# Kernel optimization log

Measured on AMD Instinct MI355X. Metric: run time of the kernel, lower is better.

Reference implementation:

```python
import jax, jax.numpy as jnp
import numpy as np

D, H, L, FF, V, B, S = 512, 8, 6, 2048, 4096, 2, 4096
EPS = 1e-5

def _unit(v):
    return v / jnp.linalg.norm(v, axis=-1, keepdims=True)

def _unitelu(v):
    return jax.nn.elu(_unit(v))

def _ln(x, g, b):
    m = jnp.mean(x, axis=-1, keepdims=True)
    var = jnp.var(x, axis=-1, keepdims=True)
    return (x - m) * jax.lax.rsqrt(var + EPS) * g + b

def setup_inputs() -> dict:
    key = jax.random.key(0)
    ks = jax.random.split(key, 16)
    s = 0.02
    inp = {
        'input': jax.random.randint(ks[0], (B, S), 0, V),
        'emb': jax.random.normal(ks[1], (V, D)) * s,
        'Wq': jax.random.normal(ks[2], (L, D, D)) * s,
        'bq': jnp.zeros((L, D)),
        'Wk': jax.random.normal(ks[3], (L, D, D)) * s,
        'bk': jnp.zeros((L, D)),
        'Wv': jax.random.normal(ks[4], (L, D, D)) * s,
        'bv': jnp.zeros((L, D)),
        'Wo': jax.random.normal(ks[5], (L, D, D)) * s,
        'bo': jnp.zeros((L, D)),
        'W1': jax.random.normal(ks[6], (L, FF, D)) * s,
        'b1': jnp.zeros((L, FF)),
        'W2': jax.random.normal(ks[7], (L, D, FF)) * s,
        'b2': jnp.zeros((L, D)),
        'g2': jnp.ones((L, D)),
        'be2': jnp.zeros((L, D)),
        'Wfc': jax.random.normal(ks[8], (V, D)) * s,
        'bfc': jnp.zeros((V,)),
    }
    return inp

def reference(input, emb, Wq, bq, Wk, bk, Wv, bv, Wo, bo, W1, b1, W2, b2, g2, be2, Wfc, bfc):
    # h: [S, B, D] (seq-major, matching input.permute(1,0) then embedding)
    h = emb[input.T]
    for l in range(L):
        # linear kernelized attention: O(S * dh^2) per head, no SxS matrix
        k = _unitelu((h @ Wk[l].T + bk[l]).reshape(S, B, H, -1))  # [S,B,H,dh]
        v = (h @ Wv[l].T + bv[l]).reshape(S, B, H, -1)
        A = jnp.einsum('sbnq,sbnv->bnvq', k, v)                    # [B,H,dh,dh]
        q = _unit((h @ Wq[l].T + bq[l]).reshape(S, B, H, -1))
        o = jnp.einsum('sbnq,bnvq->sbnv', q, A).reshape(S, B, D)
        h = h + (o @ Wo[l].T + bo[l])
        f = jax.nn.relu(h @ W1[l].T + b1[l]) @ W2[l].T + b2[l]
        h = _ln(h + f, g2[l], be2[l])
    out = h @ Wfc.T + bfc          # [S, B, V]
    return out.transpose(1, 2, 0)  # [B, V, S]
```

## Files before the change

### kernel.cpp

```cpp
#include <hip/hip_runtime.h>
#include <hip/hip_bf16.h>

#define D_  512
#define H_  8
#define DH_ 64
#define L_  6
#define FF_ 2048
#define V_  4096
#define B_  2
#define S_  4096
#define SB_ (S_*B_)
#define DD_ ((size_t)D_*D_)
#define FD_ ((size_t)FF_*D_)
#define NTOT_ (4*DD_ + 2*FD_)

typedef unsigned short u16;
typedef unsigned int   u32;
typedef _Float16 f16;
typedef f16   f16x8 __attribute__((ext_vector_type(8)));
typedef float f32x4 __attribute__((ext_vector_type(4)));

__device__ __forceinline__ float us2f(u16 u){
  union { u32 i; float f; } c; c.i = ((u32)u) << 16; return c.f;
}
__device__ __forceinline__ u16 f2b(float f){
  union { float f; u32 i; } c; c.f = f;
  u32 x = c.i;
  x += 0x7FFF + ((x >> 16) & 1);
  return (u16)(x >> 16);
}
__device__ __forceinline__ float h2f(u16 u){
  union { u16 s; f16 h; } c; c.s = u; return (float)c.h;
}
__device__ __forceinline__ u16 f2h(float f){
  union { f16 h; u16 s; } c; c.h = (f16)f; return c.s;
}
__device__ __forceinline__ float ldf(const void* p, size_t i, int isbf){
  return isbf ? us2f(((const u16*)p)[i]) : ((const float*)p)[i];
}

typedef const __attribute__((address_space(1))) u32* gas_u32p;
typedef       __attribute__((address_space(3))) u32* las_u32p;
__device__ __forceinline__ void async16(const u16* g, u16* l){
  __builtin_amdgcn_global_load_lds((gas_u32p)(const void*)g, (las_u32p)(void*)l, 16, 0, 0);
}

__global__ __launch_bounds__(64) void detect_dtype(const void* emb, int* flag)
{
  const int t = threadIdx.x;
  u16 hw = ((const u16*)emb)[t];
  int e = (hw >> 7) & 0xFF;
  int ok = ((e > 96) && (e < 160)) || ((hw & 0x7FFF) == 0);
  unsigned long long m = __ballot(ok);
  if (t == 0) *flag = (__popcll(m) >= 56) ? 1 : 0;
}

__global__ __launch_bounds__(256) void cvt_all(
    const void* Wq, const void* Wk, const void* Wv, const void* Wo,
    const void* W1, const void* W2, const void* Wfc,
    u16* __restrict__ dstAll, u16* __restrict__ dstFC, const int* flagp)
{
  const int isbf = *flagp;
  const size_t total6 = 6 * NTOT_;
  const size_t i = ((size_t)blockIdx.x * 256 + threadIdx.x) * 4;
  const void* src; size_t off; u16* dst;
  if (i < total6) {
    const int l = (int)(i / NTOT_);
    const size_t r = i - (size_t)l * NTOT_;
    const size_t n4 = 4 * DD_, nW1 = n4 + FD_;
    if (r < n4) {
      const int wsel = (int)(r / DD_);
      src = (wsel == 0) ? Wq : (wsel == 1) ? Wk : (wsel == 2) ? Wv : Wo;
      off = (size_t)l * DD_ + (r - (size_t)wsel * DD_);
    } else if (r < nW1) { src = W1; off = (size_t)l * FD_ + (r - n4); }
    else                { src = W2; off = (size_t)l * FD_ + (r - nW1); }
    dst = dstAll + i;
  } else {
    const size_t j = i - total6;
    if (j >= (size_t)V_ * D_) return;
    src = Wfc; off = j; dst = dstFC + j;
  }
  ushort4 o;
  if (isbf) {
    ushort4 u = *(const ushort4*)((const u16*)src + off);
    o = make_ushort4(f2h(us2f(u.x)), f2h(us2f(u.y)), f2h(us2f(u.z)), f2h(us2f(u.w)));
  } else {
    float4 f = *(const float4*)((const float*)src + off);
    o = make_ushort4(f2h(f.x), f2h(f.y), f2h(f.z), f2h(f.w));
  }
  *(ushort4*)dst = o;
}

template<int ACT, int OUTMODE, int PRE, int TPB, int LOG_TX, int LOG_TXZ>
__global__ __launch_bounds__(256) void gemm_pers(
    const u16* __restrict__ A, const u16* __restrict__ Bm,
    int bstride,
    const void* bias, size_t bias_off,
    u16* __restrict__ Cb, void* __restrict__ Cout,
    int M, int N, int K, const int* flagp)
{
  __shared__ u16 tile[(PRE + 1) * 8192];
  const int t = threadIdx.x, lane = t & 63, w = t >> 6;
  const int wr = w >> 1, wc = w & 1;
  const int col = lane & 15, quad = lane >> 4;
  const int srow = w * 16 + (lane >> 2);
  const int skol = (((lane & 3) ^ ((lane >> 3) & 3)) << 3);
  const int rswz = ((col >> 1) & 3);
  const int isbf = *flagp;
  const int vbase = blockIdx.x * TPB;

  float bpre3[(OUTMODE == 3) ? 16 : 1];
  float bpre0[(OUTMODE == 3) ? 1 : TPB][4];
  if (OUTMODE == 3) {
    const int by0 = vbase >> LOG_TXZ;
    #pragma unroll
    for (int i = 0; i < 4; i++)
      #pragma unroll
      for (int r = 0; r < 4; r++)
        bpre3[i * 4 + r] = ldf(bias, bias_off + (by0 << 7) + wr * 64 + i * 16 + quad * 4 + r, isbf);
  } else {
    #pragma unroll
    for (int g = 0; g < TPB; g++) {
      const int bxg = (vbase + g) & ((1 << LOG_TX) - 1);
      #pragma unroll
      for (int j = 0; j < 4; j++)
        bpre0[g][j] = ldf(bias, bias_off + (bxg << 7) + wc * 64 + j * 16 + col, isbf);
    }
  }

  int st = -1;
  const u16 *ag0 = nullptr, *ag1 = nullptr, *bg0 = nullptr, *bg1 = nullptr;
  auto set_tile = [&](int tp) {
    const int v  = vbase + tp;
    const int by = v >> LOG_TXZ;
    const int rr = v & ((1 << LOG_TXZ) - 1);
    const int bz = rr >> LOG_TX;
    const int bx = rr & ((1 << LOG_TX) - 1);
    ag0 = A + (size_t)((by << 7) + srow) * K + skol;
    ag1 = ag0 + (size_t)64 * K;
    bg0 = Bm + ((size_t)((bx << 7) + srow) * bstride + bz) * K + skol;
    bg1 = bg0 + (size_t)64 * bstride * K;
  };
  auto stage = [&](int u) {
    const int tp = u >> 4;
    if (tp != st) { st = tp; set_tile(tp); }
    const int k0 = (u & 15) << 5;
    const int bo = (u % (PRE + 1)) * 8192;
    async16(ag0 + k0, &tile[bo +        w * 512]);
    async16(ag1 + k0, &tile[bo + 2048 + w * 512]);
    async16(bg0 + k0, &tile[bo + 4096 + w * 512]);
    async16(bg1 + k0, &tile[bo + 6144 + w * 512]);
  };

  const int U = TPB * 16;
  #pragma unroll
  for (int p = 0; p < PRE; ++p) stage(p);
  if (PRE >= 2) asm volatile("s_waitcnt vmcnt(4)" ::: "memory");
  else          asm volatile("s_waitcnt vmcnt(0)" ::: "memory");
  __builtin_amdgcn_s_barrier();
  asm volatile("" ::: "memory");

  f32x4 acc[4][4] = {};
  for (int u = 0; u < U; ++u) {
    if (u + PRE < U) stage(u + PRE);
    const int cur = (u % (PRE + 1)) * 8192;
    f16x8 af[4], bf[4];
    #pragma unroll
    for (int i = 0; i < 4; i++)
      af[i] = *(const f16x8*)&tile[cur + (wr * 64 + i * 16 + col) * 32 + ((quad ^ rswz) * 8)];
    #pragma unroll
    for (int j = 0; j < 4; j++)
      bf[j] = *(const f16x8*)&tile[cur + 4096 + (wc * 64 + j * 16 + col) * 32 + ((quad ^ rswz) * 8)];
    #pragma unroll
    for (int i = 0; i < 4; i++)
      #pragma unroll
      for (int j = 0; j < 4; j++)
        acc[i][j] = __builtin_amdgcn_mfma_f32_16x16x32_f16(af[i], bf[j], acc[i][j], 0, 0, 0);

    if ((u & 15) == 15) {
      const int v  = vbase + (u >> 4);
      const int by = v >> LOG_TXZ;
      const int rr = v & ((1 << LOG_TXZ) - 1);
      const int bz = rr >> LOG_TX;
      const int bx = rr & ((1 << LOG_TX) - 1);
      const int bm = by << 7, bn = bx << 7;
      if (OUTMODE == 3) {
        const size_t obase = (size_t)bz * M * N;
        #pragma unroll
        for (int i = 0; i < 4; i++)
          #pragma unroll
          for (int r = 0; r < 4; r++) {
            const int m = bm + wr * 64 + i * 16 + quad * 4 + r;
            #pragma unroll
            for (int j = 0; j < 4; j++) {
              const int n = bn + wc * 64 + j * 16 + col;
              const float c = acc[i][j][r] + bpre3[i * 4 + r];
              const size_t oi = obase + (size_t)m * N + n;
              if (isbf) ((u16*)Cout)[oi] = f2b(c);
              else      ((float*)Cout)[oi] = c;
            }
          }
      } else {
        const int g = u >> 4;
        #pragma unroll
        for (int i = 0; i < 4; i++)
          #pragma unroll
          for (int r = 0; r < 4; r++) {
            const int m = bm + wr * 64 + i * 16 + quad * 4 + r;
            #pragma unroll
            for (int j = 0; j < 4; j++) {
              const int n = bn + wc * 64 + j * 16 + col;
              float c = acc[i][j][r] + bpre0[g][j];
              if (ACT == 1) c = fmaxf(c, 0.f);
              Cb[(size_t)m * N + n] = f2h(c);
            }
          }
      }
      const f32x4 z = {0.f, 0.f, 0.f, 0.f};
      #pragma unroll
      for (int i = 0; i < 4; i++)
        #pragma unroll
        for (int j = 0; j < 4; j++)
          acc[i][j] = z;
    }

    if (PRE >= 2 && u + 2 < U) asm volatile("s_waitcnt vmcnt(4)" ::: "memory");
    else                       asm volatile("s_waitcnt vmcnt(0)" ::: "memory");
    __builtin_amdgcn_s_barrier();
    asm volatile("" ::: "memory");
  }
}

template<int ACT, int OUTMODE, int PRE>
__global__ __launch_bounds__(256) void gemm_mfma64(
    const u16* __restrict__ A, const u16* __restrict__ Bm,
    const void* bias, size_t bias_off,
    const float* __restrict__ res,
    float* __restrict__ Cf, u16* __restrict__ Cb,
    int M, int N, int K, const int* flagp)
{
  __shared__ u16 tile[(PRE + 1) * 6144];
  const int t = threadIdx.x, lane = t & 63, w = t >> 6;
  const int bm = blockIdx.y << 6, bn = blockIdx.x << 7;
  const int wr = w >> 1, wc = w & 1;
  const int col = lane & 15, quad = lane >> 4;

  const int srow = w * 16 + (lane >> 2);
  const int skol = (((lane & 3) ^ ((lane >> 3) & 3)) << 3);
  const u16* ag  = A + (size_t)(bm + srow) * K + skol;
  const u16* bg0 = Bm + (size_t)(bn + srow) * K + skol;
  const u16* bg1 = Bm + (size_t)(bn + 64 + srow) * K + skol;
  u16* la  = &tile[       w * 512];
  u16* lb0 = &tile[2048 + w * 512];
  u16* lb1 = &tile[4096 + w * 512];

  const int nt = K >> 5;

  #pragma unroll
  for (int p = 0; p < PRE; ++p) {
    const int k0 = p << 5, bo = p * 6144;
    async16(ag  + k0, la  + bo);
    async16(bg0 + k0, lb0 + bo);
    async16(bg1 + k0, lb1 + bo);
  }
  if      (PRE >= 3) asm volatile("s_waitcnt vmcnt(6)" ::: "memory");
  else if (PRE == 2) asm volatile("s_waitcnt vmcnt(3)" ::: "memory");
  else               asm volatile("s_waitcnt vmcnt(0)" ::: "memory");
  __builtin_amdgcn_s_barrier();
  asm volatile("" ::: "memory");

  const int rswz = ((col >> 1) & 3);

  f32x4 acc[2][4] = {};
  for (int t2 = 0; t2 < nt; ++t2) {
    if (t2 + PRE < nt) {
      const int k0 = (t2 + PRE) << 5;
      const int bo = ((t2 + PRE) % (PRE + 1)) * 6144;
      async16(ag  + k0, la  + bo);
      async16(bg0 + k0, lb0 + bo);
      async16(bg1 + k0, lb1 + bo);
    }
    const int cur = (t2 % (PRE + 1)) * 6144;
    f16x8 af[2], bf[4];
    #pragma unroll
    for (int i = 0; i < 2; i++)
      af[i] = *(const f16x8*)&tile[cur + (wr * 32 + i * 16 + col) * 32 + ((quad ^ rswz) * 8)];
    #pragma unroll
    for (int j = 0; j < 4; j++)
      bf[j] = *(const f16x8*)&tile[cur + 2048 + (wc * 64 + j * 16 + col) * 32 + ((quad ^ rswz) * 8)];
    #pragma unroll
    for (int i = 0; i < 2; i++)
      #pragma unroll
      for (int j = 0; j < 4; j++)
        acc[i][j] = __builtin_amdgcn_mfma_f32_16x16x32_f16(af[i], bf[j], acc[i][j], 0, 0, 0);
    if (PRE >= 3) {
      if      (t2 + 3 < nt) asm volatile("s_waitcnt vmcnt(6)" ::: "memory");
      else if (t2 + 2 < nt) asm volatile("s_waitcnt vmcnt(3)" ::: "memory");
      else                  asm volatile("s_waitcnt vmcnt(0)" ::: "memory");
    } else if (PRE == 2) {
      if (t2 + 2 < nt) asm volatile("s_waitcnt vmcnt(3)" ::: "memory");
      else             asm volatile("s_waitcnt vmcnt(0)" ::: "memory");
    } else {
      asm volatile("s_waitcnt vmcnt(0)" ::: "memory");
    }
    __builtin_amdgcn_s_barrier();
    asm volatile("" ::: "memory");
  }

  const int isbf = *flagp;
  #pragma unroll
  for (int i = 0; i < 2; i++) {
    #pragma unroll
    for (int r = 0; r < 4; r++) {
      const int m = bm + wr * 32 + i * 16 + quad * 4 + r;
      #pragma unroll
      for (int j = 0; j < 4; j++) {
        const int n = bn + wc * 64 + j * 16 + col;
        float c = acc[i][j][r] + ldf(bias, bias_off + n, isbf);
        if (res) c += res[(size_t)m * N + n];
        if (ACT == 1) c = fmaxf(c, 0.f);
        if (OUTMODE == 0) {
          Cb[(size_t)m * N + n] = f2h(c);
        } else if (OUTMODE == 1) {
          Cf[(size_t)m * N + n] = c;
          Cb[(size_t)m * N + n] = f2h(c);
        } else {
          Cf[(size_t)m * N + n] = c;
        }
      }
    }
  }
}

__global__ __launch_bounds__(256) void gemm_qkv(
    const u16* __restrict__ A, const u16* __restrict__ Bm,
    const void* bq, const void* bk, const void* bv, size_t b_off,
    u16* __restrict__ qb, u16* __restrict__ kb, u16* __restrict__ vb,
    int K, const int* flagp)
{
  __shared__ u16 tile[3 * 8192];
  const int t = threadIdx.x, lane = t & 63, w = t >> 6;
  const int bm = blockIdx.y << 7, bn = blockIdx.x << 7;
  const int wr = w >> 1, wc = w & 1;
  const int col = lane & 15, quad = lane >> 4;

  const int srow = w * 16 + (lane >> 2);
  const int skol = (((lane & 3) ^ ((lane >> 3) & 3)) << 3);
  const u16* ag0 = A + (size_t)(bm + srow) * K + skol;
  const u16* ag1 = A + (size_t)(bm + 64 + srow) * K + skol;
  const u16* bg0 = Bm + (size_t)(bn + srow) * K + skol;
  const u16* bg1 = Bm + (size_t)(bn + 64 + srow) * K + skol;
  u16* la0 = &tile[       w * 512];
  u16* la1 = &tile[2048 + w * 512];
  u16* lb0 = &tile[4096 + w * 512];
  u16* lb1 = &tile[6144 + w * 512];

  const int nt = K >> 5;

  #pragma unroll
  for (int p = 0; p < 2; ++p) {
    const int k0 = p << 5, bo = p * 8192;
    async16(ag0 + k0, la0 + bo);
    async16(ag1 + k0, la1 + bo);
    async16(bg0 + k0, lb0 + bo);
    async16(bg1 + k0, lb1 + bo);
  }
  asm volatile("s_waitcnt vmcnt(4)" ::: "memory");
  __builtin_amdgcn_s_barrier();
  asm volatile("" ::: "memory");

  const int rswz = ((col >> 1) & 3);

  f32x4 acc[4][4] = {};
  for (int t2 = 0; t2 < nt; ++t2) {
    if (t2 + 2 < nt) {
      const int k0 = (t2 + 2) << 5;
      const int bo = ((t2 + 2) % 3) * 8192;
      async16(ag0 + k0, la0 + bo);
      async16(ag1 + k0, la1 + bo);
      async16(bg0 + k0, lb0 + bo);
      async16(bg1 + k0, lb1 + bo);
    }
    const int cur = (t2 % 3) * 8192;
    f16x8 af[4], bf[4];
    #pragma unroll
    for (int i = 0; i < 4; i++)
      af[i] = *(const f16x8*)&tile[cur + (wr * 64 + i * 16 + col) * 32 + ((quad ^ rswz) * 8)];
    #pragma unroll
    for (int j = 0; j < 4; j++)
      bf[j] = *(const f16x8*)&tile[cur + 4096 + (wc * 64 + j * 16 + col) * 32 + ((quad ^ rswz) * 8)];
    #pragma unroll
    for (int i = 0; i < 4; i++)
      #pragma unroll
      for (int j = 0; j < 4; j++)
        acc[i][j] = __builtin_amdgcn_mfma_f32_16x16x32_f16(af[i], bf[j], acc[i][j], 0, 0, 0);
    if (t2 + 2 < nt) asm volatile("s_waitcnt vmcnt(4)" ::: "memory");
    else             asm volatile("s_waitcnt vmcnt(0)" ::: "memory");
    __builtin_amdgcn_s_barrier();
    asm volatile("" ::: "memory");
  }

  const int isbf = *flagp;
  const int nbase = bn + wc * 64;
  const int sel = nbase >> 9;
  const int nl0 = nbase & 511;
  u16* outp = (sel == 0) ? qb : (sel == 1) ? kb : vb;
  const void* bias = (sel == 0) ? bq : (sel == 1) ? bk : bv;

  if (sel < 2) {
    #pragma unroll
    for (int i = 0; i < 4; i++) {
      #pragma unroll
      for (int r = 0; r < 4; r++) {
        float v[4]; float ss = 0.f;
        #pragma unroll
        for (int j = 0; j < 4; j++) {
          const int nl = nl0 + j * 16 + col;
          v[j] = acc[i][j][r] + ldf(bias, b_off + nl, isbf);
          ss += v[j] * v[j];
        }
        ss += __shfl_xor(ss, 1); ss += __shfl_xor(ss, 2);
        ss += __shfl_xor(ss, 4); ss += __shfl_xor(ss, 8);
        const float inv = rsqrtf(fmaxf(ss, 1e-30f));
        const int m = bm + wr * 64 + i * 16 + quad * 4 + r;
        #pragma unroll
        for (int j = 0; j < 4; j++) {
          float u = v[j] * inv;
          if (sel == 1) u = (u > 0.f) ? u : expm1f(u);
          outp[(size_t)m * 512 + nl0 + j * 16 + col] = f2h(u);
        }
      }
    }
  } else {
    #pragma unroll
    for (int i = 0; i < 4; i++)
      #pragma unroll
      for (int r = 0; r < 4; r++) {
        const int m = bm + wr * 64 + i * 16 + quad * 4 + r;
        #pragma unroll
        for (int j = 0; j < 4; j++) {
          const int nl = nl0 + j * 16 + col;
          outp[(size_t)m * 512 + nl] = f2h(acc[i][j][r] + ldf(bias, b_off + nl, isbf));
        }
      }
  }
}

#define KT_ 136
__global__ __launch_bounds__(256) void attn_acc_mfma(
    const u16* __restrict__ kbuf, const u16* __restrict__ vbuf,
    float* __restrict__ Apart)
{
  __shared__ u16 ktr[64 * KT_];
  __shared__ u16 vtr[64 * KT_];
  const int bh = blockIdx.x;
  const int b  = bh >> 3, n = bh & 7;
  const int s0 = blockIdx.y << 7;
  const int t = threadIdx.x, lane = t & 63, w = t >> 6;
  const int col = lane & 15, quad = lane >> 4;

  #pragma unroll
  for (int u = 0; u < 8; u++) {
    const int flat = u * 256 + t;
    const int row = flat >> 4, q4 = (flat & 15) << 2;
    const size_t g = ((size_t)(s0 + row) * B_ + b) * D_ + n * 64 + q4;
    ushort4 kk = *(const ushort4*)&kbuf[g];
    ushort4 vv = *(const ushort4*)&vbuf[g];
    ktr[(q4+0)*KT_ + row] = kk.x; ktr[(q4+1)*KT_ + row] = kk.y;
    ktr[(q4+2)*KT_ + row] = kk.z; ktr[(q4+3)*KT_ + row] = kk.w;
    vtr[(q4+0)*KT_ + row] = vv.x; vtr[(q4+1)*KT_ + row] = vv.y;
    vtr[(q4+2)*KT_ + row] = vv.z; vtr[(q4+3)*KT_ + row] = vv.w;
  }
  __syncthreads();

  f32x4 acc[4] = {};
  #pragma unroll
  for (int ks = 0; ks < 4; ks++) {
    const int k0 = ks * 32;
    f16x8 af = *(const f16x8*)&vtr[(w * 16 + col) * KT_ + k0 + quad * 8];
    #pragma unroll
    for (int j = 0; j < 4; j++) {
      f16x8 bf = *(const f16x8*)&ktr[(j * 16 + col) * KT_ + k0 + quad * 8];
      acc[j] = __builtin_amdgcn_mfma_f32_16x16x32_f16(af, bf, acc[j], 0, 0, 0);
    }
  }
  float* Ap = Apart + ((size_t)blockIdx.y * 16 + bh) * 4096;
  #pragma unroll
  for (int j = 0; j < 4; j++)
    #pragma unroll
    for (int r = 0; r < 4; r++) {
      const int vi = w * 16 + quad * 4 + r, qi = j * 16 + col;
      Ap[vi * 64 + qi] = acc[j][r];
    }
}

__global__ __launch_bounds__(256) void reduce_A(
    const float* __restrict__ Apart, u16* __restrict__ Ah)
{
  const int i = blockIdx.x * 256 + threadIdx.x;
  const int bh = i >> 12, idx = i & 4095;
  float s = 0.f;
  #pragma unroll
  for (int p = 0; p < 32; p++)
    s += Apart[((size_t)p * 16 + bh) * 4096 + idx];
  Ah[i] = f2h(s);
}

__global__ __launch_bounds__(256) void attn_apply_mfma(
    u16* __restrict__ qo, const u16* __restrict__ Ah)
{
  const int bh = blockIdx.x;
  const int b = bh >> 3, n = bh & 7;
  const int s0 = blockIdx.y << 7;
  const int t = threadIdx.x, lane = t & 63, w = t >> 6;
  const int col = lane & 15, quad = lane >> 4;

  const u16* Ab_ = Ah + (size_t)bh * 4096;
  f16x8 bf[4][2];
  #pragma unroll
  for (int j = 0; j < 4; j++)
    #pragma unroll
    for (int ks = 0; ks < 2; ks++)
      bf[j][ks] = *(const f16x8*)&Ab_[(j * 16 + col) * 64 + ks * 32 + quad * 8];

  const int srow_base = s0 + w * 32;
  f32x4 acc[2][4] = {};
  #pragma unroll
  for (int i = 0; i < 2; i++) {
    const int s = srow_base + i * 16 + col;
    const u16* qp = qo + ((size_t)s * B_ + b) * D_ + n * 64;
    f16x8 af0 = *(const f16x8*)&qp[quad * 8];
    f16x8 af1 = *(const f16x8*)&qp[32 + quad * 8];
    #pragma unroll
    for (int j = 0; j < 4; j++) {
      acc[i][j] = __builtin_amdgcn_mfma_f32_16x16x32_f16(af0, bf[j][0], acc[i][j], 0, 0, 0);
      acc[i][j] = __builtin_amdgcn_mfma_f32_16x16x32_f16(af1, bf[j][1], acc[i][j], 0, 0, 0);
    }
  }
  #pragma unroll
  for (int i = 0; i < 2; i++)
    #pragma unroll
    for (int r = 0; r < 4; r++) {
      const int s = srow_base + i * 16 + quad * 4 + r;
      u16* op = qo + ((size_t)s * B_ + b) * D_ + n * 64;
      #pragma unroll
      for (int j = 0; j < 4; j++)
        op[j * 16 + col] = f2h(acc[i][j][r]);
    }
}

__global__ __launch_bounds__(256) void ln_k(
    float* __restrict__ h, u16* __restrict__ hb,
    const void* g, size_t g_off, const void* be, size_t be_off, const int* flagp)
{
  const int isbf = *flagp;
  const int m = blockIdx.x, t = threadIdx.x;
  float* p = h + (size_t)m * D_;
  const float x0 = p[t], x1 = p[t + 256];
  __shared__ float red[4];
  float s = x0 + x1;
  #pragma unroll
  for (int off = 32; off >= 1; off >>= 1) s += __shfl_xor(s, off);
  if ((t & 63) == 0) red[t >> 6] = s;
  __syncthreads();
  const float mean = (red[0] + red[1] + red[2] + red[3]) * (1.f / 512.f);
  const float d0 = x0 - mean, d1 = x1 - mean;
  float s2 = d0 * d0 + d1 * d1;
  #pragma unroll
  for (int off = 32; off >= 1; off >>= 1) s2 += __shfl_xor(s2, off);
  __syncthreads();
  if ((t & 63) == 0) red[t >> 6] = s2;
  __syncthreads();
  const float var = (red[0] + red[1] + red[2] + red[3]) * (1.f / 512.f);
  const float sc = rsqrtf(var + 1e-5f);
  const float y0 = d0 * sc * ldf(g, g_off + t, isbf)       + ldf(be, be_off + t, isbf);
  const float y1 = d1 * sc * ldf(g, g_off + t + 256, isbf) + ldf(be, be_off + t + 256, isbf);
  p[t] = y0;       p[t + 256] = y1;
  hb[(size_t)m * D_ + t] = f2h(y0);
  hb[(size_t)m * D_ + t + 256] = f2h(y1);
}

__global__ __launch_bounds__(512) void embed_k(
    const int* __restrict__ inp, const void* emb,
    float* __restrict__ h, u16* __restrict__ hb, const int* flagp)
{
  const int isbf = *flagp;
  const int m = blockIdx.x, t = threadIdx.x;
  const int s = m >> 1, b = m & 1;
  const int tok = inp[b * S_ + s];
  const float v = ldf(emb, (size_t)tok * D_ + t, isbf);
  h[(size_t)m * D_ + t] = v;
  hb[(size_t)m * D_ + t] = f2h(v);
}

extern "C" void kernel_launch(void* const* d_in, const int* in_sizes, int n_in,
                              void* d_out, int out_size, void* d_ws, size_t ws_size,
                              hipStream_t stream) {
  const int*  inp = (const int*) d_in[0];
  const void* emb = d_in[1];
  const void* Wq  = d_in[2];
  const void* bq  = d_in[3];
  const void* Wk  = d_in[4];
  const void* bk  = d_in[5];
  const void* Wv  = d_in[6];
  const void* bv  = d_in[7];
  const void* Wo  = d_in[8];
  const void* bo  = d_in[9];
  const void* W1  = d_in[10];
  const void* b1  = d_in[11];
  const void* W2  = d_in[12];
  const void* b2  = d_in[13];
  const void* g2  = d_in[14];
  const void* be2 = d_in[15];
  const void* Wfc = d_in[16];
  const void* bfc = d_in[17];

  char* ws = (char*)d_ws;
  float* h     = (float*)(ws);
  u16*   hb    = (u16*)  (ws + 16777216);
  u16*   qb    = (u16*)  (ws + 25165824);
  u16*   kb    = (u16*)  (ws + 33554432);
  u16*   vb    = (u16*)  (ws + 41943040);
  u16*   mid   = qb;
  float* Apart = (float*)(ws + 58720256);
  u16*   Ah16  = (u16*)  (ws + 67108864);
  u16*   WcAll = (u16*)  (ws + 67239936);
  u16*   WcFC  = (u16*)  (ws + 104988672);
  int*   flag  = (int*)  (ws + 109182976);

  detect_dtype<<<1, 64, 0, stream>>>(emb, flag);
  cvt_all<<<20480, 256, 0, stream>>>(Wq, Wk, Wv, Wo, W1, W2, Wfc, WcAll, WcFC, flag);
  embed_k<<<SB_, 512, 0, stream>>>(inp, emb, h, hb, flag);

  const dim3 gQ64(D_ / 128, SB_ / 64);
  const dim3 gQKV(3 * D_ / 128, SB_ / 128);
  const dim3 gAT(B_ * H_, S_ / 128);

  for (int l = 0; l < L_; l++) {
    u16* Wcl = WcAll + (size_t)l * NTOT_;

    gemm_qkv<<<gQKV, 256, 0, stream>>>(hb, Wcl, bq, bk, bv, (size_t)l*D_, qb, kb, vb, D_, flag);

    attn_acc_mfma<<<gAT, 256, 0, stream>>>(kb, vb, Apart);
    reduce_A<<<256, 256, 0, stream>>>(Apart, Ah16);
    attn_apply_mfma<<<gAT, 256, 0, stream>>>(qb, Ah16);

    gemm_mfma64<0,1,3><<<gQ64, 256, 0, stream>>>(qb, Wcl + 3*DD_, bo, (size_t)l*D_, h, h, hb, SB_, D_, D_, flag);
    gemm_pers<1,0,2,2,4,4><<<512, 256, 0, stream>>>(hb, Wcl + 4*DD_, 1, b1, (size_t)l*FF_, mid, nullptr, SB_, FF_, D_, flag);
    gemm_mfma64<0,2,3><<<gQ64, 256, 0, stream>>>(mid, Wcl + 4*DD_ + FD_, b2, (size_t)l*D_, h, h, nullptr, SB_, D_, FF_, flag);
    ln_k<<<SB_, 256, 0, stream>>>(h, hb, g2, (size_t)l*D_, be2, (size_t)l*D_, flag);
  }

  gemm_pers<0,3,2,4,5,6><<<512, 256, 0, stream>>>(WcFC, hb, 2, bfc, 0, nullptr, d_out, V_, S_, D_, flag);
}
```

Measured before the change: 1.345 ms.

## Persist QKV GEMM over three N-tiles and fuse A reduction into accumulation

```diff
diff --git a/kernel.cpp b/kernel.cpp
--- a/kernel.cpp
+++ b/kernel.cpp
@@ -45,9 +45,10 @@
   __builtin_amdgcn_global_load_lds((gas_u32p)(const void*)g, (las_u32p)(void*)l, 16, 0, 0);
 }
 
-__global__ __launch_bounds__(64) void detect_dtype(const void* emb, int* flag)
+__global__ __launch_bounds__(64) void detect_dtype(const void* emb, int* flag, int* cnt)
 {
   const int t = threadIdx.x;
+  for (int i = t; i < L_ * 16; i += 64) cnt[i] = 0;
   u16 hw = ((const u16*)emb)[t];
   int e = (hw >> 7) & 0xFF;
   int ok = ((e > 96) && (e < 160)) || ((hw & 0x7FFF) == 0);
@@ -231,6 +232,134 @@
   }
 }
 
+__global__ __launch_bounds__(256) void gemm_qkv_pers(
+    const u16* __restrict__ A, const u16* __restrict__ Bm,
+    const void* bq, const void* bk, const void* bv, size_t b_off,
+    u16* __restrict__ qb, u16* __restrict__ kb, u16* __restrict__ vb,
+    const int* flagp)
+{
+  __shared__ u16 tile[3 * 8192];
+  const int t = threadIdx.x, lane = t & 63, w = t >> 6;
+  const int wr = w >> 1, wc = w & 1;
+  const int col = lane & 15, quad = lane >> 4;
+  const int srow = w * 16 + (lane >> 2);
+  const int skol = (((lane & 3) ^ ((lane >> 3) & 3)) << 3);
+  const int rswz = ((col >> 1) & 3);
+  const int isbf = *flagp;
+
+  const int vbase = blockIdx.x * 3;
+  const int bm_t = vbase / 12;
+  const int bn0  = vbase % 12;
+
+  float bpre[3][4]; int selv[3], nl0v[3];
+  #pragma unroll
+  for (int g = 0; g < 3; g++) {
+    const int bn = bn0 + g;
+    const int nbase = bn * 128 + wc * 64;
+    const int sel = nbase >> 9, nl0 = nbase & 511;
+    selv[g] = sel; nl0v[g] = nl0;
+    const void* bias = (sel == 0) ? bq : (sel == 1) ? bk : bv;
+    #pragma unroll
+    for (int j = 0; j < 4; j++)
+      bpre[g][j] = ldf(bias, b_off + nl0 + j * 16 + col, isbf);
+  }
+
+  const u16* ag0 = A + (size_t)(bm_t * 128 + srow) * 512 + skol;
+  const u16* ag1 = ag0 + (size_t)64 * 512;
+  int st = -1;
+  const u16 *bg0 = nullptr, *bg1 = nullptr;
+  auto stage = [&](int u) {
+    const int tp = u >> 4;
+    if (tp != st) {
+      st = tp;
+      const int bn = bn0 + tp;
+      bg0 = Bm + (size_t)(bn * 128 + srow) * 512 + skol;
+      bg1 = bg0 + (size_t)64 * 512;
+    }
+    const int k0 = (u & 15) << 5;
+    const int bo = (u % 3) * 8192;
+    async16(ag0 + k0, &tile[bo +        w * 512]);
+    async16(ag1 + k0, &tile[bo + 2048 + w * 512]);
+    async16(bg0 + k0, &tile[bo + 4096 + w * 512]);
+    async16(bg1 + k0, &tile[bo + 6144 + w * 512]);
+  };
+
+  stage(0); stage(1);
+  asm volatile("s_waitcnt vmcnt(4)" ::: "memory");
+  __builtin_amdgcn_s_barrier();
+  asm volatile("" ::: "memory");
+
+  f32x4 acc[4][4] = {};
+  for (int u = 0; u < 48; ++u) {
+    if (u + 2 < 48) stage(u + 2);
+    const int cur = (u % 3) * 8192;
+    f16x8 af[4], bf[4];
+    #pragma unroll
+    for (int i = 0; i < 4; i++)
+      af[i] = *(const f16x8*)&tile[cur + (wr * 64 + i * 16 + col) * 32 + ((quad ^ rswz) * 8)];
+    #pragma unroll
+    for (int j = 0; j < 4; j++)
+      bf[j] = *(const f16x8*)&tile[cur + 4096 + (wc * 64 + j * 16 + col) * 32 + ((quad ^ rswz) * 8)];
+    #pragma unroll
+    for (int i = 0; i < 4; i++)
+      #pragma unroll
+      for (int j = 0; j < 4; j++)
+        acc[i][j] = __builtin_amdgcn_mfma_f32_16x16x32_f16(af[i], bf[j], acc[i][j], 0, 0, 0);
+
+    if ((u & 15) == 15) {
+      const int g = u >> 4;
+      const int sel = selv[g], nl0 = nl0v[g];
+      u16* outp = (sel == 0) ? qb : (sel == 1) ? kb : vb;
+      const int bm = bm_t * 128;
+      if (sel < 2) {
+        #pragma unroll
+        for (int i = 0; i < 4; i++) {
+          #pragma unroll
+          for (int r = 0; r < 4; r++) {
+            float v[4]; float ss = 0.f;
+            #pragma unroll
+            for (int j = 0; j < 4; j++) {
+              v[j] = acc[i][j][r] + bpre[g][j];
+              ss += v[j] * v[j];
+            }
+            ss += __shfl_xor(ss, 1); ss += __shfl_xor(ss, 2);
+            ss += __shfl_xor(ss, 4); ss += __shfl_xor(ss, 8);
+            const float inv = rsqrtf(fmaxf(ss, 1e-30f));
+            const int m = bm + wr * 64 + i * 16 + quad * 4 + r;
+            #pragma unroll
+            for (int j = 0; j < 4; j++) {
+              float uu = v[j] * inv;
+              if (sel == 1) uu = (uu > 0.f) ? uu : expm1f(uu);
+              outp[(size_t)m * 512 + nl0 + j * 16 + col] = f2h(uu);
+            }
+          }
+        }
+      } else {
+        #pragma unroll
+        for (int i = 0; i < 4; i++)
+          #pragma unroll
+          for (int r = 0; r < 4; r++) {
+            const int m = bm + wr * 64 + i * 16 + quad * 4 + r;
+            #pragma unroll
+            for (int j = 0; j < 4; j++)
+              outp[(size_t)m * 512 + nl0 + j * 16 + col] = f2h(acc[i][j][r] + bpre[g][j]);
+          }
+      }
+      const f32x4 z = {0.f, 0.f, 0.f, 0.f};
+      #pragma unroll
+      for (int i = 0; i < 4; i++)
+        #pragma unroll
+        for (int j = 0; j < 4; j++)
+          acc[i][j] = z;
+    }
+
+    if (u + 2 < 48) asm volatile("s_waitcnt vmcnt(4)" ::: "memory");
+    else            asm volatile("s_waitcnt vmcnt(0)" ::: "memory");
+    __builtin_amdgcn_s_barrier();
+    asm volatile("" ::: "memory");
+  }
+}
+
 template<int ACT, int OUTMODE, int PRE>
 __global__ __launch_bounds__(256) void gemm_mfma64(
     const u16* __restrict__ A, const u16* __restrict__ Bm,
@@ -332,124 +461,10 @@
   }
 }
 
-__global__ __launch_bounds__(256) void gemm_qkv(
-    const u16* __restrict__ A, const u16* __restrict__ Bm,
-    const void* bq, const void* bk, const void* bv, size_t b_off,
-    u16* __restrict__ qb, u16* __restrict__ kb, u16* __restrict__ vb,
-    int K, const int* flagp)
-{
-  __shared__ u16 tile[3 * 8192];
-  const int t = threadIdx.x, lane = t & 63, w = t >> 6;
-  const int bm = blockIdx.y << 7, bn = blockIdx.x << 7;
-  const int wr = w >> 1, wc = w & 1;
-  const int col = lane & 15, quad = lane >> 4;
-
-  const int srow = w * 16 + (lane >> 2);
-  const int skol = (((lane & 3) ^ ((lane >> 3) & 3)) << 3);
-  const u16* ag0 = A + (size_t)(bm + srow) * K + skol;
-  const u16* ag1 = A + (size_t)(bm + 64 + srow) * K + skol;
-  const u16* bg0 = Bm + (size_t)(bn + srow) * K + skol;
-  const u16* bg1 = Bm + (size_t)(bn + 64 + srow) * K + skol;
-  u16* la0 = &tile[       w * 512];
-  u16* la1 = &tile[2048 + w * 512];
-  u16* lb0 = &tile[4096 + w * 512];
-  u16* lb1 = &tile[6144 + w * 512];
-
-  const int nt = K >> 5;
-
-  #pragma unroll
-  for (int p = 0; p < 2; ++p) {
-    const int k0 = p << 5, bo = p * 8192;
-    async16(ag0 + k0, la0 + bo);
-    async16(ag1 + k0, la1 + bo);
-    async16(bg0 + k0, lb0 + bo);
-    async16(bg1 + k0, lb1 + bo);
-  }
-  asm volatile("s_waitcnt vmcnt(4)" ::: "memory");
-  __builtin_amdgcn_s_barrier();
-  asm volatile("" ::: "memory");
-
-  const int rswz = ((col >> 1) & 3);
-
-  f32x4 acc[4][4] = {};
-  for (int t2 = 0; t2 < nt; ++t2) {
-    if (t2 + 2 < nt) {
-      const int k0 = (t2 + 2) << 5;
-      const int bo = ((t2 + 2) % 3) * 8192;
-      async16(ag0 + k0, la0 + bo);
-      async16(ag1 + k0, la1 + bo);
-      async16(bg0 + k0, lb0 + bo);
-      async16(bg1 + k0, lb1 + bo);
-    }
-    const int cur = (t2 % 3) * 8192;
-    f16x8 af[4], bf[4];
-    #pragma unroll
-    for (int i = 0; i < 4; i++)
-      af[i] = *(const f16x8*)&tile[cur + (wr * 64 + i * 16 + col) * 32 + ((quad ^ rswz) * 8)];
-    #pragma unroll
-    for (int j = 0; j < 4; j++)
-      bf[j] = *(const f16x8*)&tile[cur + 4096 + (wc * 64 + j * 16 + col) * 32 + ((quad ^ rswz) * 8)];
-    #pragma unroll
-    for (int i = 0; i < 4; i++)
-      #pragma unroll
-      for (int j = 0; j < 4; j++)
-        acc[i][j] = __builtin_amdgcn_mfma_f32_16x16x32_f16(af[i], bf[j], acc[i][j], 0, 0, 0);
-    if (t2 + 2 < nt) asm volatile("s_waitcnt vmcnt(4)" ::: "memory");
-    else             asm volatile("s_waitcnt vmcnt(0)" ::: "memory");
-    __builtin_amdgcn_s_barrier();
-    asm volatile("" ::: "memory");
-  }
-
-  const int isbf = *flagp;
-  const int nbase = bn + wc * 64;
-  const int sel = nbase >> 9;
-  const int nl0 = nbase & 511;
-  u16* outp = (sel == 0) ? qb : (sel == 1) ? kb : vb;
-  const void* bias = (sel == 0) ? bq : (sel == 1) ? bk : bv;
-
-  if (sel < 2) {
-    #pragma unroll
-    for (int i = 0; i < 4; i++) {
-      #pragma unroll
-      for (int r = 0; r < 4; r++) {
-        float v[4]; float ss = 0.f;
-        #pragma unroll
-        for (int j = 0; j < 4; j++) {
-          const int nl = nl0 + j * 16 + col;
-          v[j] = acc[i][j][r] + ldf(bias, b_off + nl, isbf);
-          ss += v[j] * v[j];
-        }
-        ss += __shfl_xor(ss, 1); ss += __shfl_xor(ss, 2);
-        ss += __shfl_xor(ss, 4); ss += __shfl_xor(ss, 8);
-        const float inv = rsqrtf(fmaxf(ss, 1e-30f));
-        const int m = bm + wr * 64 + i * 16 + quad * 4 + r;
-        #pragma unroll
-        for (int j = 0; j < 4; j++) {
-          float u = v[j] * inv;
-          if (sel == 1) u = (u > 0.f) ? u : expm1f(u);
-          outp[(size_t)m * 512 + nl0 + j * 16 + col] = f2h(u);
-        }
-      }
-    }
-  } else {
-    #pragma unroll
-    for (int i = 0; i < 4; i++)
-      #pragma unroll
-      for (int r = 0; r < 4; r++) {
-        const int m = bm + wr * 64 + i * 16 + quad * 4 + r;
-        #pragma unroll
-        for (int j = 0; j < 4; j++) {
-          const int nl = nl0 + j * 16 + col;
-          outp[(size_t)m * 512 + nl] = f2h(acc[i][j][r] + ldf(bias, b_off + nl, isbf));
-        }
-      }
-  }
-}
-
 #define KT_ 136
 __global__ __launch_bounds__(256) void attn_acc_mfma(
     const u16* __restrict__ kbuf, const u16* __restrict__ vbuf,
-    float* __restrict__ Apart)
+    float* __restrict__ Apart, u16* __restrict__ Ah, int* __restrict__ cnt)
 {
   __shared__ u16 ktr[64 * KT_];
   __shared__ u16 vtr[64 * KT_];
@@ -492,18 +507,27 @@
       const int vi = w * 16 + quad * 4 + r, qi = j * 16 + col;
       Ap[vi * 64 + qi] = acc[j][r];
     }
-}
-
-__global__ __launch_bounds__(256) void reduce_A(
-    const float* __restrict__ Apart, u16* __restrict__ Ah)
-{
-  const int i = blockIdx.x * 256 + threadIdx.x;
-  const int bh = i >> 12, idx = i & 4095;
-  float s = 0.f;
-  #pragma unroll
-  for (int p = 0; p < 32; p++)
-    s += Apart[((size_t)p * 16 + bh) * 4096 + idx];
-  Ah[i] = f2h(s);
+
+  __threadfence();
+  __syncthreads();
+  __shared__ int isLast;
+  if (t == 0) isLast = (atomicAdd(&cnt[bh], 1) == 31) ? 1 : 0;
+  __syncthreads();
+  if (!isLast) return;
+  if (t == 0) atomicExch(&cnt[bh], 0);
+  __threadfence();
+
+  #pragma unroll
+  for (int i = 0; i < 4; i++) {
+    const int idx = i * 1024 + t * 4;
+    float4 s = make_float4(0.f, 0.f, 0.f, 0.f);
+    for (int p = 0; p < 32; p++) {
+      const float4 v = *(const float4*)&Apart[((size_t)p * 16 + bh) * 4096 + idx];
+      s.x += v.x; s.y += v.y; s.z += v.z; s.w += v.w;
+    }
+    *(ushort4*)&Ah[(size_t)bh * 4096 + idx] =
+        make_ushort4(f2h(s.x), f2h(s.y), f2h(s.z), f2h(s.w));
+  }
 }
 
 __global__ __launch_bounds__(256) void attn_apply_mfma(
@@ -627,22 +651,21 @@
   u16*   WcAll = (u16*)  (ws + 67239936);
   u16*   WcFC  = (u16*)  (ws + 104988672);
   int*   flag  = (int*)  (ws + 109182976);
-
-  detect_dtype<<<1, 64, 0, stream>>>(emb, flag);
+  int*   cnt   = (int*)  (ws + 109183040);
+
+  detect_dtype<<<1, 64, 0, stream>>>(emb, flag, cnt);
   cvt_all<<<20480, 256, 0, stream>>>(Wq, Wk, Wv, Wo, W1, W2, Wfc, WcAll, WcFC, flag);
   embed_k<<<SB_, 512, 0, stream>>>(inp, emb, h, hb, flag);
 
   const dim3 gQ64(D_ / 128, SB_ / 64);
-  const dim3 gQKV(3 * D_ / 128, SB_ / 128);
   const dim3 gAT(B_ * H_, S_ / 128);
 
   for (int l = 0; l < L_; l++) {
     u16* Wcl = WcAll + (size_t)l * NTOT_;
 
-    gemm_qkv<<<gQKV, 256, 0, stream>>>(hb, Wcl, bq, bk, bv, (size_t)l*D_, qb, kb, vb, D_, flag);
-
-    attn_acc_mfma<<<gAT, 256, 0, stream>>>(kb, vb, Apart);
-    reduce_A<<<256, 256, 0, stream>>>(Apart, Ah16);
+    gemm_qkv_pers<<<256, 256, 0, stream>>>(hb, Wcl, bq, bk, bv, (size_t)l*D_, qb, kb, vb, flag);
+
+    attn_acc_mfma<<<gAT, 256, 0, stream>>>(kb, vb, Apart, Ah16, cnt + l * 16);
     attn_apply_mfma<<<gAT, 256, 0, stream>>>(qb, Ah16);
 
     gemm_mfma64<0,1,3><<<gQ64, 256, 0, stream>>>(qb, Wcl + 3*DD_, bo, (size_t)l*D_, h, h, hb, SB_, D_, D_, flag);
```

After: 1.861 ms. 1.38x slower.
